# Optimization experiments

Hardware: AMD Instinct MI355X
Metric: run time of the kernel (lower is better)

The kernel has to match this reference:

```python
import jax, jax.numpy as jnp
import numpy as np

N_NODES = 50000
N_EDGES = 1200000
IN_FEATS = 64
OUT_FEATS = 64
NEG_SLOPE = 0.01  # F.leaky_relu default


def setup_inputs() -> dict:
    key = jax.random.key(0)
    k1, k2, k3, k4, k5, k6 = jax.random.split(key, 6)
    feature = jax.random.normal(k1, (N_NODES, IN_FEATS), dtype=jnp.float32)
    attn_w = jax.random.normal(k2, (2 * IN_FEATS, 1), dtype=jnp.float32) * 0.1
    lin_w = jax.random.normal(k3, (OUT_FEATS, 2 * IN_FEATS), dtype=jnp.float32) * 0.1
    lin_b = jax.random.normal(k4, (OUT_FEATS,), dtype=jnp.float32) * 0.1
    src = jax.random.randint(k5, (N_EDGES,), 0, N_NODES, dtype=jnp.int32)
    dst = jax.random.randint(k6, (N_EDGES,), 0, N_NODES, dtype=jnp.int32)
    return {"feature": feature, "attn_w": attn_w, "lin_w": lin_w,
            "lin_b": lin_b, "src": src, "dst": dst}


def reference(feature, attn_w, lin_w, lin_b, src, dst):
    N = feature.shape[0]
    # edge attention: leaky_relu(attn_fc([h_src, h_dst]))
    # split attn weight to avoid materializing the [E, 2*in] concat
    a_src, a_dst = attn_w[:IN_FEATS, 0], attn_w[IN_FEATS:, 0]
    e = jax.nn.leaky_relu(feature[src] @ a_src + feature[dst] @ a_dst,
                          negative_slope=NEG_SLOPE)  # [E]
    # segment softmax over incoming edges of each destination node
    emax = jax.ops.segment_max(e, dst, num_segments=N)
    emax = jnp.where(jnp.isfinite(emax), emax, 0.0)  # guard empty segments
    ex = jnp.exp(e - emax[dst])                       # [E]
    denom = jax.ops.segment_sum(ex, dst, num_segments=N)          # [N]
    num = jax.ops.segment_sum(ex[:, None] * feature[src], dst,
                              num_segments=N)                      # [N, in]
    hm = jnp.where(denom[:, None] > 0, num / denom[:, None], 0.0)
    # node apply: relu(Linear([h, hm]))
    h = jnp.concatenate([feature, hm], axis=1) @ lin_w.T + lin_b
    return jax.nn.relu(h)
```

## Files before the change

kernel.cpp:

```cpp
#include <hip/hip_runtime.h>
#include <math.h>

#define N_NODES 50000
#define N_EDGES 1200000
#define F 64
#define CAP 49
#define BSTR2 56
#define OVF_MAX 1024
#define NBIN 782
#define BSTR 16
#define CAP_BIN 2304
#define TILE 8192
#define NTILE ((N_EDGES + TILE - 1) / TILE)
#define XSTR 72

typedef __attribute__((ext_vector_type(8))) short short8;
typedef __attribute__((ext_vector_type(8))) unsigned short ushort8_t;
typedef __attribute__((ext_vector_type(4))) float v4f;


__device__ __forceinline__ unsigned short f32_to_bf16_rne(float f) {
    unsigned u = __float_as_uint(f);
    return (unsigned short)((u + 0x7FFFu + ((u >> 16) & 1u)) >> 16);
}
__device__ __forceinline__ float bf16_to_f32(unsigned short u) {
    return __uint_as_float(((unsigned)u) << 16);
}

__global__ void k_prep(const float* __restrict__ feature,
                       const float* __restrict__ attn_w,
                       float* __restrict__ s, float* __restrict__ dd,
                       unsigned short* __restrict__ fb) {
    int gid = blockIdx.x * blockDim.x + threadIdx.x;
    int wave = gid >> 6;
    int lane = threadIdx.x & 63;
    if (wave >= N_NODES) return;
    float f = feature[wave * F + lane];
    fb[wave * F + lane] = f32_to_bf16_rne(f);
    float sv = f * attn_w[lane];
    float dv = f * attn_w[F + lane];
    #pragma unroll
    for (int o = 32; o > 0; o >>= 1) {
        sv += __shfl_down(sv, o, 64);
        dv += __shfl_down(dv, o, 64);
    }
    if (lane == 0) {
        s[wave] = sv;
        dd[wave] = dv;
    }
}

__global__ __launch_bounds__(256) void k_bin(
        const int* __restrict__ src, const int* __restrict__ dst,
        int* __restrict__ bin_cnt, unsigned* __restrict__ binned) {
    __shared__ unsigned ord[TILE];
    __shared__ int cnt_l[NBIN], off_l[NBIN], cur_l[NBIN], base_g[NBIN];
    __shared__ int buf[256];
    int t = threadIdx.x;
    int e0 = blockIdx.x * TILE;
    int ecnt = N_EDGES - e0; if (ecnt > TILE) ecnt = TILE;
    for (int i = t; i < NBIN; i += 256) cnt_l[i] = 0;
    __syncthreads();
    int n4 = ecnt >> 2;
    const int4* s4p = (const int4*)src + (e0 >> 2);
    const int4* d4p = (const int4*)dst + (e0 >> 2);
    unsigned pk[32];
    int ng = 0;
    #pragma unroll
    for (int k = 0; k < 8; k++) {
        int c = t + k * 256;
        if (c < n4) {
            int4 d4 = d4p[c];
            int4 s4 = s4p[c];
            pk[4 * k + 0] = (((unsigned)d4.x) << 16) | (unsigned)s4.x;
            pk[4 * k + 1] = (((unsigned)d4.y) << 16) | (unsigned)s4.y;
            pk[4 * k + 2] = (((unsigned)d4.z) << 16) | (unsigned)s4.z;
            pk[4 * k + 3] = (((unsigned)d4.w) << 16) | (unsigned)s4.w;
            atomicAdd(&cnt_l[pk[4 * k + 0] >> 22], 1);
            atomicAdd(&cnt_l[pk[4 * k + 1] >> 22], 1);
            atomicAdd(&cnt_l[pk[4 * k + 2] >> 22], 1);
            atomicAdd(&cnt_l[pk[4 * k + 3] >> 22], 1);
            ng = k + 1;
        }
    }
    __syncthreads();
    int c0[4];
    int sum = 0;
    #pragma unroll
    for (int j = 0; j < 4; j++) {
        int idx = t * 4 + j;
        c0[j] = (idx < NBIN) ? cnt_l[idx] : 0;
        sum += c0[j];
    }
    buf[t] = sum;
    __syncthreads();
    #pragma unroll
    for (int d = 1; d < 256; d <<= 1) {
        int x = (t >= d) ? buf[t - d] : 0;
        __syncthreads();
        buf[t] += x;
        __syncthreads();
    }
    int excl = buf[t] - sum;
    #pragma unroll
    for (int j = 0; j < 4; j++) {
        int idx = t * 4 + j;
        if (idx < NBIN) {
            off_l[idx] = excl;
            cur_l[idx] = excl;
            base_g[idx] = atomicAdd(&bin_cnt[idx * BSTR], c0[j]);
        }
        excl += c0[j];
    }
    __syncthreads();
    for (int k = 0; k < ng; k++) {
        #pragma unroll
        for (int u = 0; u < 4; u++) {
            unsigned v = pk[4 * k + u];
            int r = atomicAdd(&cur_l[v >> 22], 1);
            ord[r] = v;
        }
    }
    __syncthreads();
    for (int i = t; i < ecnt; i += 256) {
        unsigned v = ord[i];
        int b = v >> 22;
        int pos = base_g[b] + (i - off_l[b]);
        if (pos < CAP_BIN) binned[(size_t)b * CAP_BIN + pos] = v;
    }
}

__global__ __launch_bounds__(256, 4) void k_fused(
        const unsigned* __restrict__ binned, const int* __restrict__ bin_cnt,
        int* __restrict__ cnt, unsigned short* __restrict__ bucket,
        int* __restrict__ ovf_cnt, unsigned* __restrict__ ovf,
        const float* __restrict__ s, const float* __restrict__ dd,
        const unsigned short* __restrict__ fb,
        const float* __restrict__ lin_w, const float* __restrict__ lin_b,
        float* __restrict__ out) {
    __shared__ int cnt_l[64];
    __shared__ __align__(16) unsigned short buck_l[64 * BSTR2];
    __shared__ unsigned short Wl[64 * 136];
    __shared__ __align__(16) unsigned short xl[4][16][XSTR];
    __shared__ __align__(16) float p_l[4][64];
    int t = threadIdx.x;
    int wid = t >> 6, lane = t & 63;
    int bin = blockIdx.x;
    int n0 = bin << 6;
    int nn = N_NODES - n0; if (nn > 64) nn = 64;
    for (int i = t; i < 64 * 128; i += 256)
        Wl[(i >> 7) * 136 + (i & 127)] = f32_to_bf16_rne(lin_w[i]);
    if (t < 64) cnt_l[t] = 0;
    {
        uint4 z4 = {0, 0, 0, 0};
        uint4* b4 = (uint4*)buck_l;
        for (int i = t; i < 448; i += 256) b4[i] = z4;
    }
    __syncthreads();
    int E = bin_cnt[bin * BSTR];
    if (E > CAP_BIN) E = CAP_BIN;
    const unsigned* be = binned + (size_t)bin * CAP_BIN;
    for (int i = t; i < E; i += 256) {
        unsigned v = be[i];
        int local = (v >> 16) & 63;
        int sid = (int)(v & 0xFFFFu);
        int r = atomicAdd(&cnt_l[local], 1);
        if (r < CAP) {
            buck_l[local * BSTR2 + r] = (unsigned short)sid;
        } else {
            int o = atomicAdd(ovf_cnt, 1);
            if (o < OVF_MAX)
                ovf[o] = ((unsigned)(n0 + local) << 16) | (unsigned)sid;
        }
    }
    __syncthreads();
    if (t < nn) {
        cnt[n0 + t] = cnt_l[t];
        if (cnt_l[t] > CAP) {
            for (int k2 = 0; k2 < CAP; k2++)
                bucket[(size_t)(n0 + t) * CAP + k2] = buck_l[t * BSTR2 + k2];
        }
    }
    __syncthreads();
    const ushort4* f4 = (const ushort4*)fb;
    int grp = lane >> 4;
    int c16 = lane & 15;
    for (int j = 0; j < 16; j++) {
        int local = wid * 16 + j;
        if (local >= nn) break;
        int deg = cnt_l[local];
        if (deg == 0 || deg > CAP) {
            if (lane < 16) {
                ushort4 z = {0, 0, 0, 0};
                *(ushort4*)&xl[wid][j][lane * 4] = z;
            }
            continue;
        }
        float pr = 0.0f;
        if (lane < deg) {
            int si = (int)buck_l[local * BSTR2 + lane];
            float v = s[si] + dd[n0 + local];
            v = v > 0.0f ? v : 0.01f * v;
            pr = __expf(v);
        }
        float l = pr;
        #pragma unroll
        for (int o = 32; o > 0; o >>= 1)
            l += __shfl_xor(l, o, 64);
        p_l[wid][lane] = pr * __builtin_amdgcn_rcpf(l);
        float a0 = 0.0f, a1 = 0.0f, a2 = 0.0f, a3 = 0.0f;
        for (int e0 = 0; e0 < deg; e0 += 32) {
            ushort8_t skv = *(const ushort8_t*)
                &buck_l[local * BSTR2 + e0 + grp * 8];
            float4 pA = *(const float4*)&p_l[wid][e0 + grp * 8];
            float4 pB = *(const float4*)&p_l[wid][e0 + grp * 8 + 4];
            ushort4 fv[8];
            #pragma unroll
            for (int u = 0; u < 8; u++)
                fv[u] = f4[(int)skv[u] * 16 + c16];
            float pw[8] = {pA.x, pA.y, pA.z, pA.w, pB.x, pB.y, pB.z, pB.w};
            #pragma unroll
            for (int u = 0; u < 8; u++) {
                a0 = fmaf(pw[u], bf16_to_f32(fv[u].x), a0);
                a1 = fmaf(pw[u], bf16_to_f32(fv[u].y), a1);
                a2 = fmaf(pw[u], bf16_to_f32(fv[u].z), a2);
                a3 = fmaf(pw[u], bf16_to_f32(fv[u].w), a3);
            }
        }
        a0 += __shfl_xor(a0, 16, 64); a0 += __shfl_xor(a0, 32, 64);
        a1 += __shfl_xor(a1, 16, 64); a1 += __shfl_xor(a1, 32, 64);
        a2 += __shfl_xor(a2, 16, 64); a2 += __shfl_xor(a2, 32, 64);
        a3 += __shfl_xor(a3, 16, 64); a3 += __shfl_xor(a3, 32, 64);
        if (lane < 16) {
            ushort4 st;
            st.x = f32_to_bf16_rne(a0);
            st.y = f32_to_bf16_rne(a1);
            st.z = f32_to_bf16_rne(a2);
            st.w = f32_to_bf16_rne(a3);
            *(ushort4*)&xl[wid][j][c16 * 4] = st;
        }
    }
    int n0w = n0 + wid * 16;
    if (n0w >= N_NODES) return;
    int m = lane & 15, quad = lane >> 4;
    short8 afr[4];
    #pragma unroll
    for (int ks = 0; ks < 2; ks++) {
        int kb = ks * 32 + quad * 8;
        afr[ks] = *(const short8*)&fb[(size_t)(n0w + m) * F + kb];
    }
    #pragma unroll
    for (int ks = 2; ks < 4; ks++) {
        int kb = (ks - 2) * 32 + quad * 8;
        afr[ks] = *(const short8*)&xl[wid][m][kb];
    }
    #pragma unroll
    for (int nt = 0; nt < 4; nt++) {
        v4f acc = {0.0f, 0.0f, 0.0f, 0.0f};
        #pragma unroll
        for (int ks = 0; ks < 4; ks++) {
            int kb = ks * 32 + quad * 8;
            short8 b = *(const short8*)&Wl[(nt * 16 + m) * 136 + kb];
            acc = __builtin_amdgcn_mfma_f32_16x16x32_bf16(afr[ks], b, acc,
                                                          0, 0, 0);
        }
        int colo = nt * 16 + m;
        float bias = lin_b[colo];
        #pragma unroll
        for (int r = 0; r < 4; r++) {
            int row = quad * 4 + r;
            float v = acc[r] + bias;
            out[(size_t)(n0w + row) * F + colo] = fmaxf(v, 0.0f);
        }
    }
}

__global__ __launch_bounds__(256) void k_cleanup(
        const unsigned short* __restrict__ bucket,
        const int* __restrict__ cnt,
        const int* __restrict__ ovf_cnt, const unsigned int* __restrict__ ovf,
        const float* __restrict__ s, const float* __restrict__ dd,
        const float* __restrict__ feature,
        const float* __restrict__ lin_w, const float* __restrict__ lin_b,
        float* __restrict__ out) {
    int M = *ovf_cnt;
    if (M > OVF_MAX) M = OVF_MAX;
    if (M == 0) return;
    __shared__ float Wl[64 * 129];
    __shared__ int list[128];
    __shared__ int nlist;
    __shared__ unsigned short edg[4][256];
    __shared__ float xc[4][128];
    int t = threadIdx.x;
    for (int i = t; i < 64 * 128; i += 256)
        Wl[(i >> 7) * 129 + (i & 127)] = lin_w[i];
    if (t == 0) {
        nlist = 0;
        for (int i = 0; i < M; i++) {
            int d = (int)(ovf[i] >> 16);
            bool seen = false;
            for (int j = 0; j < nlist; j++) if (list[j] == d) seen = true;
            if (!seen && nlist < 128) list[nlist++] = d;
        }
    }
    __syncthreads();
    int wid = t >> 6, lane = t & 63;
    for (int idx = wid; idx < nlist; idx += 4) {
        int n = list[idx];
        int deg = cnt[n];
        if (lane < CAP) edg[wid][lane] = bucket[n * CAP + lane];
        int k2 = CAP;
        for (int base = 0; base < M; base += 64) {
            int i2 = base + lane;
            unsigned val = 0;
            bool mt = false;
            if (i2 < M) { val = ovf[i2]; mt = ((int)(val >> 16) == n); }
            unsigned long long mask = __ballot(mt);
            if (mt) {
                int pos = k2 + __popcll(mask & ((1ULL << lane) - 1ULL));
                if (pos < 256) edg[wid][pos] = (unsigned short)(val & 0xFFFFu);
            }
            k2 += __popcll(mask);
        }
        __threadfence_block();
        int nd = deg < 256 ? deg : 256;
        float m = -1e30f, l = 0.0f, acc = 0.0f;
        float dn = dd[n];
        for (int c0 = 0; c0 < nd; c0 += 64) {
            int j = c0 + lane;
            int sid = 0;
            float ev = -1e30f;
            if (j < nd) {
                sid = (int)edg[wid][j];
                float v = s[sid] + dn;
                ev = v > 0.0f ? v : 0.01f * v;
            }
            float cm = ev;
            #pragma unroll
            for (int o = 32; o > 0; o >>= 1)
                cm = fmaxf(cm, __shfl_xor(cm, o, 64));
            float np = (j < nd) ? __expf(ev - cm) : 0.0f;
            float cl = np;
            #pragma unroll
            for (int o = 32; o > 0; o >>= 1)
                cl += __shfl_xor(cl, o, 64);
            float cacc = 0.0f;
            int c = nd - c0; if (c > 64) c = 64;
            for (int k = 0; k < c; k += 16) {
                float fvv[16];
                #pragma unroll
                for (int u = 0; u < 16; u++) {
                    int sk = __builtin_amdgcn_readlane(sid, k + u);
                    fvv[u] = feature[sk * F + lane];
                }
                #pragma unroll
                for (int u = 0; u < 16; u++) {
                    float pk = __uint_as_float(
                        __builtin_amdgcn_readlane(__float_as_uint(np), k + u));
                    cacc = fmaf(pk, fvv[u], cacc);
                }
            }
            float mn = fmaxf(m, cm);
            float sc = __expf(m - mn);
            float sc2 = __expf(cm - mn);
            l = l * sc + cl * sc2;
            acc = acc * sc + cacc * sc2;
            m = mn;
        }
        float hm = acc / l;
        xc[wid][lane] = feature[n * F + lane];
        xc[wid][64 + lane] = hm;
        __threadfence_block();
        float oa = lin_b[lane];
        #pragma unroll
        for (int k = 0; k < 128; k++)
            oa += xc[wid][k] * Wl[lane * 129 + k];
        out[n * F + lane] = fmaxf(oa, 0.0f);
    }
}

extern "C" void kernel_launch(void* const* d_in, const int* in_sizes, int n_in,
                              void* d_out, int out_size, void* d_ws, size_t ws_size,
                              hipStream_t stream) {
    const float* feature = (const float*)d_in[0];
    const float* attn_w  = (const float*)d_in[1];
    const float* lin_w   = (const float*)d_in[2];
    const float* lin_b   = (const float*)d_in[3];
    const int*   src     = (const int*)d_in[4];
    const int*   dst     = (const int*)d_in[5];
    float* out = (float*)d_out;
    char* ws = (char*)d_ws;

    float*          s       = (float*)(ws);
    float*          dd      = (float*)(ws + 200000);
    int*            cnt     = (int*)  (ws + 400000);
    int*            bin_cnt = (int*)  (ws + 600000);
    int*            ovf_cnt = (int*)  (ws + 650048);
    unsigned*       ovf     = (unsigned*)(ws + 650112);
    unsigned short* bucket  = (unsigned short*)(ws + 654208);
    unsigned*       binned  = (unsigned*)(ws + 5554208);
    unsigned short* fb      = (unsigned short*)(ws + 12761120);

    hipMemsetAsync(ws + 600000, 0, 50112, stream);
    k_prep<<<(N_NODES * 64) / 256, 256, 0, stream>>>(
        feature, attn_w, s, dd, fb);
    k_bin<<<NTILE, 256, 0, stream>>>(src, dst, bin_cnt, binned);
    k_fused<<<NBIN, 256, 0, stream>>>(
        binned, bin_cnt, cnt, bucket, ovf_cnt, ovf, s, dd, fb,
        lin_w, lin_b, out);
    k_cleanup<<<1, 256, 0, stream>>>(
        bucket, cnt, ovf_cnt, ovf, s, dd, feature, lin_w, lin_b, out);
}
```

Baseline: 142.3 us.

## Gather neighbor features as FP8 and merge prep with binning kernel

Adds an FP8 (packed four per 32-bit word) copy of the node features and uses it for the edge-weighted neighbor aggregation gather instead of bf16, halving bytes per random gather. It also folds the per-node prep work into extra blocks of the edge-binning kernel so the two run in one launch and can overlap. FP8 quantization of features reduces accuracy of the aggregated messages, which risks exceeding tolerance.

```diff
diff --git a/kernel.cpp b/kernel.cpp
--- a/kernel.cpp
+++ b/kernel.cpp
@@ -15,7 +15,6 @@
 #define XSTR 72
 
 typedef __attribute__((ext_vector_type(8))) short short8;
-typedef __attribute__((ext_vector_type(8))) unsigned short ushort8_t;
 typedef __attribute__((ext_vector_type(4))) float v4f;
 
 
@@ -23,40 +22,43 @@
     unsigned u = __float_as_uint(f);
     return (unsigned short)((u + 0x7FFFu + ((u >> 16) & 1u)) >> 16);
 }
-__device__ __forceinline__ float bf16_to_f32(unsigned short u) {
-    return __uint_as_float(((unsigned)u) << 16);
-}
-
-__global__ void k_prep(const float* __restrict__ feature,
-                       const float* __restrict__ attn_w,
-                       float* __restrict__ s, float* __restrict__ dd,
-                       unsigned short* __restrict__ fb) {
-    int gid = blockIdx.x * blockDim.x + threadIdx.x;
-    int wave = gid >> 6;
-    int lane = threadIdx.x & 63;
-    if (wave >= N_NODES) return;
-    float f = feature[wave * F + lane];
-    fb[wave * F + lane] = f32_to_bf16_rne(f);
-    float sv = f * attn_w[lane];
-    float dv = f * attn_w[F + lane];
-    #pragma unroll
-    for (int o = 32; o > 0; o >>= 1) {
-        sv += __shfl_down(sv, o, 64);
-        dv += __shfl_down(dv, o, 64);
-    }
-    if (lane == 0) {
-        s[wave] = sv;
-        dd[wave] = dv;
-    }
-}
-
-__global__ __launch_bounds__(256) void k_bin(
+
+__global__ __launch_bounds__(256) void k_prep_bin(
         const int* __restrict__ src, const int* __restrict__ dst,
-        int* __restrict__ bin_cnt, unsigned* __restrict__ binned) {
+        int* __restrict__ bin_cnt, unsigned* __restrict__ binned,
+        const float* __restrict__ feature, const float* __restrict__ attn_w,
+        float* __restrict__ s, float* __restrict__ dd,
+        unsigned short* __restrict__ fb, unsigned* __restrict__ fq32) {
     __shared__ unsigned ord[TILE];
     __shared__ int cnt_l[NBIN], off_l[NBIN], cur_l[NBIN], base_g[NBIN];
     __shared__ int buf[256];
     int t = threadIdx.x;
+    if (blockIdx.x >= NTILE) {
+        int wave = (int)(blockIdx.x - NTILE) * 4 + (t >> 6);
+        int lane = t & 63;
+        if (wave >= N_NODES) return;
+        float f = feature[wave * F + lane];
+        fb[wave * F + lane] = f32_to_bf16_rne(f);
+        float g0 = __shfl(f, (lane * 4 + 0) & 63, 64);
+        float g1 = __shfl(f, (lane * 4 + 1) & 63, 64);
+        float g2 = __shfl(f, (lane * 4 + 2) & 63, 64);
+        float g3 = __shfl(f, (lane * 4 + 3) & 63, 64);
+        int pk0 = __builtin_amdgcn_cvt_pk_fp8_f32(g0, g1, 0, false);
+        int pkw = __builtin_amdgcn_cvt_pk_fp8_f32(g2, g3, pk0, true);
+        if (lane < 16) fq32[wave * 16 + lane] = (unsigned)pkw;
+        float sv = f * attn_w[lane];
+        float dv = f * attn_w[F + lane];
+        #pragma unroll
+        for (int o = 32; o > 0; o >>= 1) {
+            sv += __shfl_down(sv, o, 64);
+            dv += __shfl_down(dv, o, 64);
+        }
+        if (lane == 0) {
+            s[wave] = sv;
+            dd[wave] = dv;
+        }
+        return;
+    }
     int e0 = blockIdx.x * TILE;
     int ecnt = N_EDGES - e0; if (ecnt > TILE) ecnt = TILE;
     for (int i = t; i < NBIN; i += 256) cnt_l[i] = 0;
@@ -135,7 +137,7 @@
         int* __restrict__ cnt, unsigned short* __restrict__ bucket,
         int* __restrict__ ovf_cnt, unsigned* __restrict__ ovf,
         const float* __restrict__ s, const float* __restrict__ dd,
-        const unsigned short* __restrict__ fb,
+        const unsigned short* __restrict__ fb, const unsigned* __restrict__ fq32,
         const float* __restrict__ lin_w, const float* __restrict__ lin_b,
         float* __restrict__ out) {
     __shared__ int cnt_l[64];
@@ -182,7 +184,6 @@
         }
     }
     __syncthreads();
-    const ushort4* f4 = (const ushort4*)fb;
     int grp = lane >> 4;
     int c16 = lane & 15;
     for (int j = 0; j < 16; j++) {
@@ -210,21 +211,22 @@
         p_l[wid][lane] = pr * __builtin_amdgcn_rcpf(l);
         float a0 = 0.0f, a1 = 0.0f, a2 = 0.0f, a3 = 0.0f;
         for (int e0 = 0; e0 < deg; e0 += 32) {
-            ushort8_t skv = *(const ushort8_t*)
-                &buck_l[local * BSTR2 + e0 + grp * 8];
+            ushort4 skA = *(const ushort4*)&buck_l[local * BSTR2 + e0 + grp * 8];
+            ushort4 skB = *(const ushort4*)&buck_l[local * BSTR2 + e0 + grp * 8 + 4];
             float4 pA = *(const float4*)&p_l[wid][e0 + grp * 8];
             float4 pB = *(const float4*)&p_l[wid][e0 + grp * 8 + 4];
-            ushort4 fv[8];
+            unsigned wv[8];
+            int sk[8] = {skA.x, skA.y, skA.z, skA.w, skB.x, skB.y, skB.z, skB.w};
             #pragma unroll
             for (int u = 0; u < 8; u++)
-                fv[u] = f4[(int)skv[u] * 16 + c16];
+                wv[u] = fq32[sk[u] * 16 + c16];
             float pw[8] = {pA.x, pA.y, pA.z, pA.w, pB.x, pB.y, pB.z, pB.w};
             #pragma unroll
             for (int u = 0; u < 8; u++) {
-                a0 = fmaf(pw[u], bf16_to_f32(fv[u].x), a0);
-                a1 = fmaf(pw[u], bf16_to_f32(fv[u].y), a1);
-                a2 = fmaf(pw[u], bf16_to_f32(fv[u].z), a2);
-                a3 = fmaf(pw[u], bf16_to_f32(fv[u].w), a3);
+                a0 = fmaf(pw[u], __builtin_amdgcn_cvt_f32_fp8(wv[u], 0), a0);
+                a1 = fmaf(pw[u], __builtin_amdgcn_cvt_f32_fp8(wv[u], 1), a1);
+                a2 = fmaf(pw[u], __builtin_amdgcn_cvt_f32_fp8(wv[u], 2), a2);
+                a3 = fmaf(pw[u], __builtin_amdgcn_cvt_f32_fp8(wv[u], 3), a3);
             }
         }
         a0 += __shfl_xor(a0, 16, 64); a0 += __shfl_xor(a0, 32, 64);
@@ -400,13 +402,13 @@
     unsigned short* bucket  = (unsigned short*)(ws + 654208);
     unsigned*       binned  = (unsigned*)(ws + 5554208);
     unsigned short* fb      = (unsigned short*)(ws + 12761120);
+    unsigned*       fq32    = (unsigned*)(ws + 19161120);
 
     hipMemsetAsync(ws + 600000, 0, 50112, stream);
-    k_prep<<<(N_NODES * 64) / 256, 256, 0, stream>>>(
-        feature, attn_w, s, dd, fb);
-    k_bin<<<NTILE, 256, 0, stream>>>(src, dst, bin_cnt, binned);
+    k_prep_bin<<<NTILE + (N_NODES + 3) / 4, 256, 0, stream>>>(
+        src, dst, bin_cnt, binned, feature, attn_w, s, dd, fb, fq32);
     k_fused<<<NBIN, 256, 0, stream>>>(
-        binned, bin_cnt, cnt, bucket, ovf_cnt, ovf, s, dd, fb,
+        binned, bin_cnt, cnt, bucket, ovf_cnt, ovf, s, dd, fb, fq32,
         lin_w, lin_b, out);
     k_cleanup<<<1, 256, 0, stream>>>(
         bucket, cnt, ovf_cnt, ovf, s, dd, feature, lin_w, lin_b, out);
```

Measured after the change: 145.3 us. 1.02x slower.
